# Optimization experiments

Measured on AMD Instinct MI355X. Metric: run time of the kernel, lower is better.

The kernel has to match this reference:

```python
import jax, jax.numpy as jnp
import numpy as np

GAMMA = 1.0
MAX_SIMILARITY = 1.0


def setup_inputs() -> dict:
    key = jax.random.key(0)
    k1, k2, k3 = jax.random.split(key, 3)
    B, Ns, D = 64, 1024, 256
    d_vectors = jax.random.normal(k1, (B, Ns, D), dtype=jnp.float32)
    S = jax.random.uniform(k2, (Ns, Ns), dtype=jnp.float32)  # MinMax-normalized sims in [0,1]
    W = (jax.random.uniform(k3, (Ns, Ns)) > 0.3).astype(jnp.float32)  # binary mask (simmat > 0)
    return {"d_vectors": d_vectors, "S": S, "W": W}


def reference(d_vectors, S, W):
    B, Ns, D = d_vectors.shape
    eye = jnp.eye(Ns, dtype=d_vectors.dtype)
    # pairwise L2 distances via ||a-b||^2 = |a|^2 + |b|^2 - 2 a.b  (batched GEMM)
    sq = jnp.sum(d_vectors * d_vectors, axis=-1)                     # [B, Ns]
    G = jnp.einsum('bnd,bmd->bnm', d_vectors, d_vectors)             # [B, Ns, Ns]
    dist2 = jnp.maximum(sq[:, :, None] + sq[:, None, :] - 2.0 * G, 0.0)
    # diagonal of Kd is zeroed below; offset it so sqrt is safe (output unchanged)
    dist = jnp.sqrt(dist2 + eye[None])
    Kd = jnp.exp(-GAMMA * dist)                                      # gram matrix [B, Ns, Ns]
    Kd_tilde = Kd * (1.0 - eye)                                      # Kd - Kd*I
    S_tilde = S - MAX_SIMILARITY * eye                               # [Ns, Ns]
    diff = W[None] * (Kd_tilde - S_tilde[None])
    numer = jnp.sqrt(jnp.sum(diff * diff, axis=(1, 2)))              # per-batch Frobenius norm
    denom = jnp.sqrt(jnp.sum((W - eye) ** 2))
    return jnp.sum(2.0 * numer / denom)
```

## Files before the change

kernel.cpp:

```cpp
#include <hip/hip_runtime.h>
#include <hip/hip_bf16.h>

#define NB 64
#define NS 1024
#define DD 256
#define NT 36
#define THR 120.0f

typedef __attribute__((ext_vector_type(4))) float f32x4;
typedef __attribute__((ext_vector_type(8))) short bf16x8;
typedef __attribute__((ext_vector_type(8))) unsigned short u16x8;
typedef __attribute__((ext_vector_type(4))) unsigned short u16x4;

__device__ __forceinline__ unsigned short f2bf(float x) {
  union { float f; unsigned int u; } c; c.f = x;
  unsigned int r = c.u + 0x7fffu + ((c.u >> 16) & 1u);
  return (unsigned short)(r >> 16);
}


__global__ __launch_bounds__(256) void prep_kernel(const float* __restrict__ din,
                                                   unsigned short* __restrict__ dbf2,
                                                   float* __restrict__ sq,
                                                   const float* __restrict__ S,
                                                   const float* __restrict__ W,
                                                   float* __restrict__ dpart,
                                                   float* __restrict__ cpart,
                                                   int write_bf) {
  const int px = (int)blockIdx.x;
  const int wid = (int)threadIdx.x >> 6;
  const int l = (int)threadIdx.x & 63;
  if (px < 1024) {
    __shared__ unsigned short lds[4][16][256];
    unsigned short (*T)[256] = lds[wid];
    const int tb = (px & 7) * 128 + (px >> 3);
    const int task = tb * 4 + wid;
    const int b = task >> 6, rt = task & 63;
    const float4* src =
        reinterpret_cast<const float4*>(din + ((size_t)b * NS + rt * 16) * DD) + l;
    #pragma unroll
    for (int r16 = 0; r16 < 16; ++r16) {
      float4 v = src[r16 * 64];
      float s = v.x * v.x + v.y * v.y + v.z * v.z + v.w * v.w;
      #pragma unroll
      for (int off = 32; off > 0; off >>= 1) s += __shfl_xor(s, off, 64);
      if (l == 0) sq[(size_t)b * NS + rt * 16 + r16] = s;
      if (write_bf) {
        u16x4 o;
        o[0] = f2bf(v.x); o[1] = f2bf(v.y); o[2] = f2bf(v.z); o[3] = f2bf(v.w);
        const int cp = (l >> 1) ^ (r16 & 7);
        *reinterpret_cast<u16x4*>(&T[r16][cp * 8 + (l & 1) * 4]) = o;
      }
    }
    if (write_bf) {
      unsigned short* dst = dbf2 + (((size_t)b * 8) * 64 + rt) * 512 + (size_t)l * 8;
      #pragma unroll
      for (int kg = 0; kg < 8; ++kg) {
        const int cc = (kg * 4 + (l >> 4)) ^ (l & 7);
        u16x8 frag = *reinterpret_cast<const u16x8*>(&T[l & 15][cc * 8]);
        *reinterpret_cast<u16x8*>(dst + (size_t)kg * 64 * 512) = frag;
      }
    }
    return;
  }
  const int blk = px - 1024;
  const int base = blk * 256 + (int)threadIdx.x;
  float dsum = 0.f, csum = 0.f;
  #pragma unroll
  for (int rpt = 0; rpt < 2; ++rpt) {
    const int idx = base + rpt * 131072;
    float4 w = reinterpret_cast<const float4*>(W)[idx];
    float4 s4 = reinterpret_cast<const float4*>(S)[idx];
    const int e0 = idx << 2;
    const int r = e0 >> 10, c0 = e0 & 1023;
    float wv[4] = {w.x, w.y, w.z, w.w};
    float sv[4] = {s4.x, s4.y, s4.z, s4.w};
    #pragma unroll
    for (int i = 0; i < 4; ++i) {
      const bool dg = (c0 + i) == r;
      const float a = wv[i] - (dg ? 1.0f : 0.0f);
      dsum = fmaf(a, a, dsum);
      const float bq = dg ? (1.0f - sv[i]) : sv[i];
      csum = fmaf(wv[i] * bq, bq, csum);
    }
  }
  #pragma unroll
  for (int off = 32; off > 0; off >>= 1) {
    dsum += __shfl_xor(dsum, off, 64);
    csum += __shfl_xor(csum, off, 64);
  }
  __shared__ float redD[4], redC[4];
  if (l == 0) { redD[wid] = dsum; redC[wid] = csum; }
  __syncthreads();
  if (threadIdx.x == 0) {
    dpart[blk] = redD[0] + redD[1] + redD[2] + redD[3];
    cpart[blk] = redC[0] + redC[1] + redC[2] + redC[3];
  }
}

template <int MODE>
__global__ __launch_bounds__(256, 2) void main_kernel(
    const float* __restrict__ dvec, const unsigned short* __restrict__ dbf2,
    const float* __restrict__ sq, const float* __restrict__ S,
    const float* __restrict__ W, float* __restrict__ npart) {
  const int tid = threadIdx.x;
  const int lane = tid & 63;
  const int wid = tid >> 6;
  const int wr = wid >> 1;
  const int wc = wid & 1;

  const int orig = (int)blockIdx.x;
  const int bid = (orig & 7) * (NT * NB / 8) + (orig >> 3);
  const int t = bid % NT;
  const int b = bid / NT;
  int u = t, ti = 0;
  while (u >= 8 - ti) { u -= 8 - ti; ++ti; }
  const int tj = ti + u;
  const int brow = ti * 128;
  const int bcol = tj * 128;

  const int rtA0 = ti * 8 + wr * 4;
  const int rtB0 = tj * 8 + wc * 4;

  f32x4 acc[4][4];
  #pragma unroll
  for (int m = 0; m < 4; ++m)
    #pragma unroll
    for (int n = 0; n < 4; ++n) acc[m][n] = f32x4{0.f, 0.f, 0.f, 0.f};

  if (MODE == 0) {
    const unsigned short* pa =
        dbf2 + (((size_t)b * 8) * 64 + rtA0) * 512 + (size_t)lane * 8;
    const unsigned short* pb =
        dbf2 + (((size_t)b * 8) * 64 + rtB0) * 512 + (size_t)lane * 8;
    bf16x8 af[4], bf[4], nf[4];
    #pragma unroll
    for (int m = 0; m < 4; ++m)
      af[m] = *reinterpret_cast<const bf16x8*>(pa + m * 512);
    #pragma unroll
    for (int n = 0; n < 4; ++n)
      bf[n] = *reinterpret_cast<const bf16x8*>(pb + n * 512);
    #pragma unroll
    for (int kg = 0; kg < 8; ++kg) {
      if (kg < 7) {
        #pragma unroll
        for (int m = 0; m < 4; ++m)
          nf[m] = *reinterpret_cast<const bf16x8*>(pa + 32768 + m * 512);
      }
      #pragma unroll
      for (int n = 0; n < 4; ++n) {
        #pragma unroll
        for (int m = 0; m < 4; ++m)
          acc[m][n] = __builtin_amdgcn_mfma_f32_16x16x32_bf16(af[m], bf[n], acc[m][n], 0, 0, 0);
        if (kg < 7)
          bf[n] = *reinterpret_cast<const bf16x8*>(pb + 32768 + n * 512);
      }
      if (kg < 7) {
        #pragma unroll
        for (int m = 0; m < 4; ++m) af[m] = nf[m];
        pa += 32768; pb += 32768;
      }
    }
  } else {
    const float* pbase = dvec + (size_t)b * NS * DD + (lane >> 4) * 8;
    #pragma unroll
    for (int kg = 0; kg < 8; ++kg) {
      bf16x8 af[4], bf[4];
      #pragma unroll
      for (int m = 0; m < 4; ++m) {
        const float* p = pbase + (size_t)((rtA0 + m) * 16 + (lane & 15)) * DD + kg * 32;
        float4 v0 = reinterpret_cast<const float4*>(p)[0];
        float4 v1 = reinterpret_cast<const float4*>(p)[1];
        af[m][0] = (short)f2bf(v0.x); af[m][1] = (short)f2bf(v0.y);
        af[m][2] = (short)f2bf(v0.z); af[m][3] = (short)f2bf(v0.w);
        af[m][4] = (short)f2bf(v1.x); af[m][5] = (short)f2bf(v1.y);
        af[m][6] = (short)f2bf(v1.z); af[m][7] = (short)f2bf(v1.w);
      }
      #pragma unroll
      for (int n = 0; n < 4; ++n) {
        const float* p = pbase + (size_t)((rtB0 + n) * 16 + (lane & 15)) * DD + kg * 32;
        float4 v0 = reinterpret_cast<const float4*>(p)[0];
        float4 v1 = reinterpret_cast<const float4*>(p)[1];
        bf[n][0] = (short)f2bf(v0.x); bf[n][1] = (short)f2bf(v0.y);
        bf[n][2] = (short)f2bf(v0.z); bf[n][3] = (short)f2bf(v0.w);
        bf[n][4] = (short)f2bf(v1.x); bf[n][5] = (short)f2bf(v1.y);
        bf[n][6] = (short)f2bf(v1.z); bf[n][7] = (short)f2bf(v1.w);
      }
      #pragma unroll
      for (int m = 0; m < 4; ++m)
        #pragma unroll
        for (int n = 0; n < 4; ++n)
          acc[m][n] = __builtin_amdgcn_mfma_f32_16x16x32_bf16(af[m], bf[n], acc[m][n], 0, 0, 0);
    }
  }

  const float* sqb = sq + (size_t)b * NS;
  const int hi = lane >> 4, lo = lane & 15;
  float sqc[4];
  #pragma unroll
  for (int n = 0; n < 4; ++n) sqc[n] = sqb[bcol + wc * 64 + n * 16 + lo];
  float dmin = 1e30f;
  #pragma unroll
  for (int m = 0; m < 4; ++m) {
    #pragma unroll
    for (int j = 0; j < 4; ++j) {
      const int r = brow + wr * 64 + m * 16 + hi * 4 + j;
      const float sqr = sqb[r];
      #pragma unroll
      for (int n = 0; n < 4; ++n) {
        const int c = bcol + wc * 64 + n * 16 + lo;
        const float d2 = fmaxf(sqr + sqc[n] - 2.0f * acc[m][n][j], 0.0f);
        dmin = fminf(dmin, (r < c) ? d2 : 1e30f);
      }
    }
  }
  float wsum = 0.f;
  if (__any(dmin < THR)) {
    float lsum = 0.f;
    #pragma unroll
    for (int m = 0; m < 4; ++m) {
      #pragma unroll
      for (int j = 0; j < 4; ++j) {
        const int r = brow + wr * 64 + m * 16 + hi * 4 + j;
        const float sqr = sqb[r];
        #pragma unroll
        for (int n = 0; n < 4; ++n) {
          const int c = bcol + wc * 64 + n * 16 + lo;
          const float d2 = fmaxf(sqr + sqc[n] - 2.0f * acc[m][n][j], 0.0f);
          if ((r < c) && (d2 < THR)) {
            const float kd = __expf(-sqrtf(d2));
            const float wrc = W[(size_t)r * NS + c];
            const float wcr = W[(size_t)c * NS + r];
            const float src_ = S[(size_t)r * NS + c];
            const float scr = S[(size_t)c * NS + r];
            lsum = fmaf(kd, kd * (wrc + wcr) - 2.0f * fmaf(wrc, src_, wcr * scr), lsum);
          }
        }
      }
    }
    #pragma unroll
    for (int off = 32; off > 0; off >>= 1) lsum += __shfl_xor(lsum, off, 64);
    wsum = lsum;
  }
  if (lane == 0) npart[(size_t)bid * 4 + wid] = wsum;
}

__global__ void final_kernel(const float* __restrict__ npart,
                             const float* __restrict__ dpart,
                             const float* __restrict__ cpart,
                             float* __restrict__ out) {
  const int lane = threadIdx.x;
  float dsum = 0.f, csum = 0.f;
  #pragma unroll
  for (int j = 0; j < 8; ++j) {
    dsum += dpart[lane + 64 * j];
    csum += cpart[lane + 64 * j];
  }
  #pragma unroll
  for (int off = 32; off > 0; off >>= 1) {
    dsum += __shfl_xor(dsum, off, 64);
    csum += __shfl_xor(csum, off, 64);
  }
  float nb = 0.f;
  const f32x4* np = reinterpret_cast<const f32x4*>(npart + (size_t)lane * 144);
  #pragma unroll
  for (int j = 0; j < 36; ++j) {
    f32x4 v = np[j];
    nb += v[0] + v[1] + v[2] + v[3];
  }
  float v = 2.0f * sqrtf(csum + nb);
  #pragma unroll
  for (int off = 32; off > 0; off >>= 1) v += __shfl_xor(v, off, 64);
  if (lane == 0) out[0] = v / sqrtf(dsum);
}

extern "C" void kernel_launch(void* const* d_in, const int* in_sizes, int n_in,
                              void* d_out, int out_size, void* d_ws, size_t ws_size,
                              hipStream_t stream) {
  const float* dvec = (const float*)d_in[0];
  const float* S = (const float*)d_in[1];
  const float* W = (const float*)d_in[2];
  float* out = (float*)d_out;

  const size_t bf_bytes = (size_t)NB * NS * DD * sizeof(unsigned short);
  const size_t sq_bytes = (size_t)NB * NS * sizeof(float);
  const size_t small_bytes = sq_bytes + (9216 + 512 + 512) * sizeof(float);
  const bool full = ws_size >= bf_bytes + small_bytes;

  unsigned short* dbf2;
  float* sqp;
  if (full) {
    dbf2 = (unsigned short*)d_ws;
    sqp = (float*)((char*)d_ws + bf_bytes);
  } else {
    dbf2 = nullptr;
    sqp = (float*)d_ws;
  }
  float* npart = sqp + (size_t)NB * NS;
  float* dpart = npart + 9216;
  float* cpart = dpart + 512;

  prep_kernel<<<1024 + 512, 256, 0, stream>>>(dvec, dbf2, sqp, S, W, dpart, cpart,
                                              full ? 1 : 0);
  if (full)
    main_kernel<0><<<NT * NB, 256, 0, stream>>>(dvec, dbf2, sqp, S, W, npart);
  else
    main_kernel<1><<<NT * NB, 256, 0, stream>>>(dvec, dbf2, sqp, S, W, npart);
  final_kernel<<<1, 64, 0, stream>>>(npart, dpart, cpart, out);
}
```

Before: 48.08 us.

## Split prep into smaller blocks and move S/W reduction into main kernel tail

The prep kernel now runs 4096 blocks of 128 threads. Each block handles one 16-row tile, with two waves cooperating through shared LDS, where before each 256-thread wave did its own tile. The S/W constant reductions (dpart/cpart) leave the prep kernel and run as 512 extra blocks appended to the main kernel grid. The goal is finer-grained parallelism and a shorter prep kernel. The extra blocks fill the tail of the main kernel, but the new __syncthreads in prep adds some overhead.

```diff
diff --git a/kernel.cpp b/kernel.cpp
--- a/kernel.cpp
+++ b/kernel.cpp
@@ -19,82 +19,42 @@
 }
 
 
-__global__ __launch_bounds__(256) void prep_kernel(const float* __restrict__ din,
+__global__ __launch_bounds__(128) void prep_kernel(const float* __restrict__ din,
                                                    unsigned short* __restrict__ dbf2,
                                                    float* __restrict__ sq,
-                                                   const float* __restrict__ S,
-                                                   const float* __restrict__ W,
-                                                   float* __restrict__ dpart,
-                                                   float* __restrict__ cpart,
                                                    int write_bf) {
+  __shared__ unsigned short T[16][256];
   const int px = (int)blockIdx.x;
   const int wid = (int)threadIdx.x >> 6;
   const int l = (int)threadIdx.x & 63;
-  if (px < 1024) {
-    __shared__ unsigned short lds[4][16][256];
-    unsigned short (*T)[256] = lds[wid];
-    const int tb = (px & 7) * 128 + (px >> 3);
-    const int task = tb * 4 + wid;
-    const int b = task >> 6, rt = task & 63;
-    const float4* src =
-        reinterpret_cast<const float4*>(din + ((size_t)b * NS + rt * 16) * DD) + l;
-    #pragma unroll
-    for (int r16 = 0; r16 < 16; ++r16) {
-      float4 v = src[r16 * 64];
-      float s = v.x * v.x + v.y * v.y + v.z * v.z + v.w * v.w;
-      #pragma unroll
-      for (int off = 32; off > 0; off >>= 1) s += __shfl_xor(s, off, 64);
-      if (l == 0) sq[(size_t)b * NS + rt * 16 + r16] = s;
-      if (write_bf) {
-        u16x4 o;
-        o[0] = f2bf(v.x); o[1] = f2bf(v.y); o[2] = f2bf(v.z); o[3] = f2bf(v.w);
-        const int cp = (l >> 1) ^ (r16 & 7);
-        *reinterpret_cast<u16x4*>(&T[r16][cp * 8 + (l & 1) * 4]) = o;
-      }
-    }
+  const int tb = (px & 7) * 512 + (px >> 3);
+  const int b = tb >> 6, rt = tb & 63;
+  const float4* src =
+      reinterpret_cast<const float4*>(din + ((size_t)b * NS + rt * 16) * DD) + l;
+  #pragma unroll
+  for (int j = 0; j < 8; ++j) {
+    const int ri = wid * 8 + j;
+    float4 v = src[ri * 64];
+    float s = v.x * v.x + v.y * v.y + v.z * v.z + v.w * v.w;
+    #pragma unroll
+    for (int off = 32; off > 0; off >>= 1) s += __shfl_xor(s, off, 64);
+    if (l == 0) sq[(size_t)b * NS + rt * 16 + ri] = s;
     if (write_bf) {
-      unsigned short* dst = dbf2 + (((size_t)b * 8) * 64 + rt) * 512 + (size_t)l * 8;
-      #pragma unroll
-      for (int kg = 0; kg < 8; ++kg) {
-        const int cc = (kg * 4 + (l >> 4)) ^ (l & 7);
-        u16x8 frag = *reinterpret_cast<const u16x8*>(&T[l & 15][cc * 8]);
-        *reinterpret_cast<u16x8*>(dst + (size_t)kg * 64 * 512) = frag;
-      }
-    }
-    return;
-  }
-  const int blk = px - 1024;
-  const int base = blk * 256 + (int)threadIdx.x;
-  float dsum = 0.f, csum = 0.f;
-  #pragma unroll
-  for (int rpt = 0; rpt < 2; ++rpt) {
-    const int idx = base + rpt * 131072;
-    float4 w = reinterpret_cast<const float4*>(W)[idx];
-    float4 s4 = reinterpret_cast<const float4*>(S)[idx];
-    const int e0 = idx << 2;
-    const int r = e0 >> 10, c0 = e0 & 1023;
-    float wv[4] = {w.x, w.y, w.z, w.w};
-    float sv[4] = {s4.x, s4.y, s4.z, s4.w};
-    #pragma unroll
-    for (int i = 0; i < 4; ++i) {
-      const bool dg = (c0 + i) == r;
-      const float a = wv[i] - (dg ? 1.0f : 0.0f);
-      dsum = fmaf(a, a, dsum);
-      const float bq = dg ? (1.0f - sv[i]) : sv[i];
-      csum = fmaf(wv[i] * bq, bq, csum);
-    }
-  }
-  #pragma unroll
-  for (int off = 32; off > 0; off >>= 1) {
-    dsum += __shfl_xor(dsum, off, 64);
-    csum += __shfl_xor(csum, off, 64);
-  }
-  __shared__ float redD[4], redC[4];
-  if (l == 0) { redD[wid] = dsum; redC[wid] = csum; }
+      u16x4 o;
+      o[0] = f2bf(v.x); o[1] = f2bf(v.y); o[2] = f2bf(v.z); o[3] = f2bf(v.w);
+      const int cp = (l >> 1) ^ (ri & 7);
+      *reinterpret_cast<u16x4*>(&T[ri][cp * 8 + (l & 1) * 4]) = o;
+    }
+  }
+  if (!write_bf) return;
   __syncthreads();
-  if (threadIdx.x == 0) {
-    dpart[blk] = redD[0] + redD[1] + redD[2] + redD[3];
-    cpart[blk] = redC[0] + redC[1] + redC[2] + redC[3];
+  unsigned short* dst = dbf2 + (((size_t)b * 8) * 64 + rt) * 512 + (size_t)l * 8;
+  #pragma unroll
+  for (int q = 0; q < 4; ++q) {
+    const int kg = wid * 4 + q;
+    const int cc = (kg * 4 + (l >> 4)) ^ (l & 7);
+    u16x8 frag = *reinterpret_cast<const u16x8*>(&T[l & 15][cc * 8]);
+    *reinterpret_cast<u16x8*>(dst + (size_t)kg * 64 * 512) = frag;
   }
 }
 
@@ -102,14 +62,52 @@
 __global__ __launch_bounds__(256, 2) void main_kernel(
     const float* __restrict__ dvec, const unsigned short* __restrict__ dbf2,
     const float* __restrict__ sq, const float* __restrict__ S,
-    const float* __restrict__ W, float* __restrict__ npart) {
+    const float* __restrict__ W, float* __restrict__ npart,
+    float* __restrict__ dpart, float* __restrict__ cpart) {
   const int tid = threadIdx.x;
   const int lane = tid & 63;
   const int wid = tid >> 6;
+  const int orig = (int)blockIdx.x;
+
+  if (orig >= NT * NB) {
+    const int blk = orig - NT * NB;
+    const int base = blk * 256 + tid;
+    float dsum = 0.f, csum = 0.f;
+    #pragma unroll
+    for (int rpt = 0; rpt < 2; ++rpt) {
+      const int idx = base + rpt * 131072;
+      float4 w = reinterpret_cast<const float4*>(W)[idx];
+      float4 s4 = reinterpret_cast<const float4*>(S)[idx];
+      const int e0 = idx << 2;
+      const int r = e0 >> 10, c0 = e0 & 1023;
+      float wv[4] = {w.x, w.y, w.z, w.w};
+      float sv[4] = {s4.x, s4.y, s4.z, s4.w};
+      #pragma unroll
+      for (int i = 0; i < 4; ++i) {
+        const bool dg = (c0 + i) == r;
+        const float a = wv[i] - (dg ? 1.0f : 0.0f);
+        dsum = fmaf(a, a, dsum);
+        const float bq = dg ? (1.0f - sv[i]) : sv[i];
+        csum = fmaf(wv[i] * bq, bq, csum);
+      }
+    }
+    #pragma unroll
+    for (int off = 32; off > 0; off >>= 1) {
+      dsum += __shfl_xor(dsum, off, 64);
+      csum += __shfl_xor(csum, off, 64);
+    }
+    __shared__ float redD[4], redC[4];
+    if (lane == 0) { redD[wid] = dsum; redC[wid] = csum; }
+    __syncthreads();
+    if (tid == 0) {
+      dpart[blk] = redD[0] + redD[1] + redD[2] + redD[3];
+      cpart[blk] = redC[0] + redC[1] + redC[2] + redC[3];
+    }
+    return;
+  }
+
   const int wr = wid >> 1;
   const int wc = wid & 1;
-
-  const int orig = (int)blockIdx.x;
   const int bid = (orig & 7) * (NT * NB / 8) + (orig >> 3);
   const int t = bid % NT;
   const int b = bid / NT;
@@ -300,11 +298,12 @@
   float* dpart = npart + 9216;
   float* cpart = dpart + 512;
 
-  prep_kernel<<<1024 + 512, 256, 0, stream>>>(dvec, dbf2, sqp, S, W, dpart, cpart,
-                                              full ? 1 : 0);
+  prep_kernel<<<4096, 128, 0, stream>>>(dvec, dbf2, sqp, full ? 1 : 0);
   if (full)
-    main_kernel<0><<<NT * NB, 256, 0, stream>>>(dvec, dbf2, sqp, S, W, npart);
+    main_kernel<0><<<NT * NB + 512, 256, 0, stream>>>(dvec, dbf2, sqp, S, W,
+                                                      npart, dpart, cpart);
   else
-    main_kernel<1><<<NT * NB, 256, 0, stream>>>(dvec, dbf2, sqp, S, W, npart);
+    main_kernel<1><<<NT * NB + 512, 256, 0, stream>>>(dvec, dbf2, sqp, S, W,
+                                                      npart, dpart, cpart);
   final_kernel<<<1, 64, 0, stream>>>(npart, dpart, cpart, out);
 }
```

After: 46.57 us. 1.03x faster.
